# Optimization experiments

Measured on AMD Instinct MI355X. Metric: run time of the kernel, lower is better.

Reference implementation:

```python
import jax, jax.numpy as jnp
import numpy as np

B, S, QD, KD = 8, 8192, 1024, 1024
AD = min(QD, KD)
EPS = 1e-5


def _ste(x, xq):
    # straight-through estimator: forward uses xq, gradient flows as identity
    return x + jax.lax.stop_gradient(xq - x)


def bitlinear(x, w, b):
    """BitNet b1.58-style BitLinear: ternary per-tensor weight quant,
    per-token int8 absmax activation quant, both with STE."""
    s = jnp.mean(jnp.abs(w)) + EPS                      # per-tensor weight scale
    wq = _ste(w, jnp.clip(jnp.round(w / s), -1.0, 1.0) * s)
    g = jnp.max(jnp.abs(x), axis=-1, keepdims=True) + EPS  # per-token act scale
    xq = _ste(x, jnp.clip(jnp.round(x * (127.0 / g)), -128.0, 127.0) * (g / 127.0))
    return jnp.matmul(xq, wq.T) + b


def setup_inputs() -> dict:
    key = jax.random.key(0)
    ks = jax.random.split(key, 6)
    sc = 0.02
    return {
        "query": jax.random.normal(ks[0], (B, QD), dtype=jnp.float32),
        "context_memory": jax.random.normal(ks[1], (B, S, KD), dtype=jnp.float32),
        "w_q": jax.random.normal(ks[2], (AD, QD), dtype=jnp.float32) * sc,
        "b_q": jnp.zeros((AD,), dtype=jnp.float32),
        "w_k": jax.random.normal(ks[3], (AD, KD), dtype=jnp.float32) * sc,
        "b_k": jnp.zeros((AD,), dtype=jnp.float32),
        "w_v": jax.random.normal(ks[4], (QD, KD), dtype=jnp.float32) * sc,
        "b_v": jnp.zeros((QD,), dtype=jnp.float32),
        "w_c": jax.random.normal(ks[5], (QD, 2 * QD), dtype=jnp.float32) * sc,
        "b_c": jnp.zeros((QD,), dtype=jnp.float32),
    }


def reference(query, context_memory, w_q, b_q, w_k, b_k, w_v, b_v, w_c, b_c):
    attention_dim = w_q.shape[0]
    q = bitlinear(query, w_q, b_q)                 # [B, A]
    k = bitlinear(context_memory, w_k, b_k)        # [B, S, A]
    v = bitlinear(context_memory, w_v, b_v)        # [B, S, QD]
    scores = jnp.einsum('ba,bsa->bs', q, k) / (attention_dim ** 0.5)
    attn = jax.nn.softmax(scores, axis=-1)         # [B, S]
    ctx = jnp.einsum('bs,bsq->bq', attn, v)        # [B, QD]
    combined = jnp.concatenate([query, ctx], axis=-1)  # [B, 2*QD]
    return bitlinear(combined, w_c, b_c)           # [B, QD]
```

## Files before the change

kernel.cpp:

```cpp
#include <hip/hip_runtime.h>
#include <hip/hip_bf16.h>
#include <math.h>

#define EPS 1e-5f

static constexpr int Bb = 8;
static constexpr int Ss = 8192;
static constexpr int Dd = 1024;
static constexpr int NW = 128;
static constexpr int NWv = NW * 4;
static constexpr int TOK = Ss / NWv;
static constexpr int NCH = 64;
static constexpr int RC = Dd / NCH;


__device__ __forceinline__ float blk_reduce(float v, bool ismax, volatile float* lds) {
#pragma unroll
  for (int msk = 32; msk; msk >>= 1) {
    float o = __shfl_xor(v, msk);
    v = ismax ? fmaxf(v, o) : (v + o);
  }
  int w = threadIdx.x >> 6;
  __syncthreads();
  if ((threadIdx.x & 63) == 0) lds[w] = v;
  __syncthreads();
  return ismax ? fmaxf(fmaxf(lds[0], lds[1]), fmaxf(lds[2], lds[3]))
               : (lds[0] + lds[1] + lds[2] + lds[3]);
}

__device__ __forceinline__ float wred_max(float v) {
#pragma unroll
  for (int msk = 32; msk; msk >>= 1) v = fmaxf(v, __shfl_xor(v, msk));
  return v;
}

__device__ __forceinline__ float wred_sum(float v) {
#pragma unroll
  for (int msk = 32; msk; msk >>= 1) v += __shfl_xor(v, msk);
  return v;
}

__device__ __forceinline__ float quantf(float x, float c) {
  return fminf(fmaxf(rintf(x * c), -128.f), 127.f);
}

__device__ __forceinline__ float ternf(float w, float s) {
  return fminf(fmaxf(rintf(w / s), -1.f), 1.f);
}

__device__ __forceinline__ float4 tern4(float4 w, float s) {
  return make_float4(ternf(w.x, s), ternf(w.y, s), ternf(w.z, s), ternf(w.w, s));
}

__device__ __forceinline__ float4 quant4(float4 v, float c) {
  return make_float4(quantf(v.x, c), quantf(v.y, c), quantf(v.z, c), quantf(v.w, c));
}

__device__ __forceinline__ float absmax4(float4 v) {
  return fmaxf(fmaxf(fabsf(v.x), fabsf(v.y)), fmaxf(fabsf(v.z), fabsf(v.w)));
}


__global__ __launch_bounds__(256) void k_scales(
    const float* __restrict__ w0, const float* __restrict__ w1,
    const float* __restrict__ w2, const float* __restrict__ w3,
    double* __restrict__ part, float* __restrict__ scales, int* __restrict__ cnt)
{
  int seg = blockIdx.x >> 6;
  int blk = blockIdx.x & 63;
  const float* w = seg == 0 ? w0 : seg == 1 ? w1 : seg == 2 ? w2 : w3;
  int n4 = (seg == 3 ? (1024 * 2048) : (1024 * 1024)) >> 2;
  const float4* w4 = (const float4*)w;
  double acc = 0.0;
  for (int i = blk * 256 + threadIdx.x; i < n4; i += 64 * 256) {
    float4 v = w4[i];
    acc += (double)fabsf(v.x) + (double)fabsf(v.y)
         + (double)fabsf(v.z) + (double)fabsf(v.w);
  }
  __shared__ double sred[256];
  sred[threadIdx.x] = acc;
  __syncthreads();
  for (int s = 128; s > 0; s >>= 1) {
    if (threadIdx.x < s) sred[threadIdx.x] += sred[threadIdx.x + s];
    __syncthreads();
  }
  __shared__ int lastold;
  if (threadIdx.x == 0) {
    part[blockIdx.x] = sred[0];
    __threadfence();
    lastold = atomicAdd(cnt, 1);
  }
  __syncthreads();
  if (lastold == 255) {
    __threadfence();
    if (threadIdx.x < 4) {
      int sg = threadIdx.x;
      double s = 0.0;
      for (int i = 0; i < 64; i++) s += part[sg * 64 + i];
      double n = (sg == 3) ? 2097152.0 : 1048576.0;
      scales[sg] = (float)(s / n) + EPS;
    }
  }
}


__global__ __launch_bounds__(256) void k_qgemv(
    const float* __restrict__ query, const float* __restrict__ W,
    const float* __restrict__ bias, const float* __restrict__ scales,
    float* __restrict__ out)
{
  __shared__ float cs[Dd];
  __shared__ float red[4];
  int b = blockIdx.x >> 8, grp = blockIdx.x & 255;
  int tid = threadIdx.x, wv = tid >> 6, lane = tid & 63;
  float4 v = ((const float4*)(query + (size_t)b * Dd))[tid];
  float am = blk_reduce(absmax4(v), true, red);
  float g = am + EPS;
  float c = 127.0f / g;
  ((float4*)cs)[tid] = quant4(v, c);
  __syncthreads();
  float s = scales[0];
  int o = grp * 4 + wv;
  const float4* wr = (const float4*)(W + (size_t)o * Dd);
  float acc = 0.f;
#pragma unroll
  for (int i = 0; i < 4; i++) {
    int idx = i * 64 + lane;
    float4 w4 = wr[idx];
    float4 a4 = ((const float4*)cs)[idx];
    acc += a4.x * ternf(w4.x, s) + a4.y * ternf(w4.y, s)
         + a4.z * ternf(w4.z, s) + a4.w * ternf(w4.w, s);
  }
  acc = wred_sum(acc);
  if (lane == 0) out[(size_t)b * Dd + o] = s * (g / 127.0f) * acc + bias[o];
}


__global__ __launch_bounds__(256) void k_qk(
    const float* __restrict__ q, const float* __restrict__ Wk,
    const float* __restrict__ bk, const float* __restrict__ scales,
    float* __restrict__ part, float* __restrict__ qk, float* __restrict__ qdotbk,
    int* __restrict__ cnt)
{
  __shared__ float qs[Bb * RC];
  int ch = blockIdx.x;
  int a0 = ch * RC;
  int tid = threadIdx.x;
  if (tid < Bb * RC) {
    int b = tid / RC, a = tid - b * RC;
    qs[tid] = q[(size_t)b * Dd + a0 + a];
  }
  __syncthreads();
  float s = scales[1];
  float4 acc[Bb];
#pragma unroll
  for (int b = 0; b < Bb; b++) acc[b] = make_float4(0.f, 0.f, 0.f, 0.f);
  const float4* Wr = (const float4*)(Wk + (size_t)a0 * Dd);
  for (int i = 0; i < RC; i++) {
    float4 t4 = tern4(Wr[(size_t)i * 256 + tid], s);
#pragma unroll
    for (int b = 0; b < Bb; b++) {
      float qb = qs[b * RC + i];
      acc[b].x += qb * t4.x; acc[b].y += qb * t4.y;
      acc[b].z += qb * t4.z; acc[b].w += qb * t4.w;
    }
  }
#pragma unroll
  for (int b = 0; b < Bb; b++)
    ((float4*)part)[((size_t)ch * Bb + b) * 256 + tid] = acc[b];

  __threadfence();
  if (tid == 0) {
    atomicAdd(cnt, 1);
    while (__hip_atomic_load(cnt, __ATOMIC_ACQUIRE, __HIP_MEMORY_SCOPE_AGENT) < NCH)
      __builtin_amdgcn_s_sleep(8);
  }
  __syncthreads();
  __threadfence();

  int b = blockIdx.x >> 3, dc = blockIdx.x & 7;
  if (tid < 32) {
    int d4 = dc * 32 + tid;
    float4 a = make_float4(0.f, 0.f, 0.f, 0.f);
    for (int k = 0; k < NCH; k++) {
      float4 p = ((const float4*)part)[((size_t)k * Bb + b) * 256 + d4];
      a.x += p.x; a.y += p.y; a.z += p.z; a.w += p.w;
    }
    ((float4*)qk)[(size_t)b * 256 + d4] = make_float4(s * a.x, s * a.y, s * a.z, s * a.w);
  } else if (dc == 0 && tid >= 64 && tid < 128) {
    int lane = tid - 64;
    float p = 0.f;
    for (int a2 = lane; a2 < Dd; a2 += 64) p += q[(size_t)b * Dd + a2] * bk[a2];
    p = wred_sum(p);
    if (lane == 0) qdotbk[b] = p;
  }
}


__global__ __launch_bounds__(256) void k_pass(
    const float* __restrict__ X, const float* __restrict__ qk,
    const float* __restrict__ qdotbk,
    float* __restrict__ m_part, float* __restrict__ l_part,
    float* __restrict__ t_part)
{
  int b    = blockIdx.x >> 7;
  int wg   = blockIdx.x & 127;
  int wv   = threadIdx.x >> 6;
  int lane = threadIdx.x & 63;
  int widx = wg * 4 + wv;
  int s0   = widx * TOK;

  const float4* qkb = (const float4*)(qk + (size_t)b * Dd);
  float4 qv0 = qkb[lane], qv1 = qkb[64 + lane], qv2 = qkb[128 + lane], qv3 = qkb[192 + lane];
  float qb = qdotbk[b];
  const float4* Xw = (const float4*)(X + ((size_t)b * Ss + s0) * Dd);

  float m = -INFINITY, l = 0.f;
  float4 a0 = make_float4(0,0,0,0), a1 = a0, a2 = a0, a3 = a0;

  float4 x0 = Xw[lane], x1 = Xw[64 + lane], x2 = Xw[128 + lane], x3 = Xw[192 + lane];
  for (int i = 0; i < TOK; i++) {
    size_t nb = (size_t)((i + 1 < TOK) ? i + 1 : i) * 256;
    float4 n0 = Xw[nb + lane], n1 = Xw[nb + 64 + lane],
           n2 = Xw[nb + 128 + lane], n3 = Xw[nb + 192 + lane];

    float am = wred_max(fmaxf(fmaxf(absmax4(x0), absmax4(x1)),
                              fmaxf(absmax4(x2), absmax4(x3))));
    float g = am + EPS;
    float c = 127.0f / g;
    float gi = g / 127.0f;

    float q00 = rintf(x0.x * c), q01 = rintf(x0.y * c), q02 = rintf(x0.z * c), q03 = rintf(x0.w * c);
    float q10 = rintf(x1.x * c), q11 = rintf(x1.y * c), q12 = rintf(x1.z * c), q13 = rintf(x1.w * c);
    float q20 = rintf(x2.x * c), q21 = rintf(x2.y * c), q22 = rintf(x2.z * c), q23 = rintf(x2.w * c);
    float q30 = rintf(x3.x * c), q31 = rintf(x3.y * c), q32 = rintf(x3.z * c), q33 = rintf(x3.w * c);

    float dt = q00 * qv0.x + q01 * qv0.y + q02 * qv0.z + q03 * qv0.w
             + q10 * qv1.x + q11 * qv1.y + q12 * qv1.z + q13 * qv1.w
             + q20 * qv2.x + q21 * qv2.y + q22 * qv2.z + q23 * qv2.w
             + q30 * qv3.x + q31 * qv3.y + q32 * qv3.z + q33 * qv3.w;
    dt = wred_sum(dt);

    float score = (dt * gi + qb) * 0.03125f;
    if (score <= m) {
      float p  = __expf(score - m);
      l += p;
      float cf = p * gi;
      a0.x += cf * q00; a0.y += cf * q01; a0.z += cf * q02; a0.w += cf * q03;
      a1.x += cf * q10; a1.y += cf * q11; a1.z += cf * q12; a1.w += cf * q13;
      a2.x += cf * q20; a2.y += cf * q21; a2.z += cf * q22; a2.w += cf * q23;
      a3.x += cf * q30; a3.y += cf * q31; a3.z += cf * q32; a3.w += cf * q33;
    } else {
      float scl = __expf(m - score);
      l = l * scl + 1.0f;
      float cf = gi;
      a0.x = a0.x * scl + cf * q00; a0.y = a0.y * scl + cf * q01;
      a0.z = a0.z * scl + cf * q02; a0.w = a0.w * scl + cf * q03;
      a1.x = a1.x * scl + cf * q10; a1.y = a1.y * scl + cf * q11;
      a1.z = a1.z * scl + cf * q12; a1.w = a1.w * scl + cf * q13;
      a2.x = a2.x * scl + cf * q20; a2.y = a2.y * scl + cf * q21;
      a2.z = a2.z * scl + cf * q22; a2.w = a2.w * scl + cf * q23;
      a3.x = a3.x * scl + cf * q30; a3.y = a3.y * scl + cf * q31;
      a3.z = a3.z * scl + cf * q32; a3.w = a3.w * scl + cf * q33;
      m = score;
    }
    x0 = n0; x1 = n1; x2 = n2; x3 = n3;
  }

  size_t pidx = (size_t)b * NWv + widx;
  float4* tpw = (float4*)t_part + (size_t)pidx * 256;
  tpw[lane] = a0; tpw[64 + lane] = a1; tpw[128 + lane] = a2; tpw[192 + lane] = a3;
  if (lane == 0) { m_part[pidx] = m; l_part[pidx] = l; }
}


__global__ __launch_bounds__(256) void k_comb(
    const float* __restrict__ m_part, const float* __restrict__ l_part,
    const float* __restrict__ t_part, float* __restrict__ t16,
    float* __restrict__ t, int* __restrict__ cnt)
{
  __shared__ float red[4];
  int b = blockIdx.x >> 4, k = blockIdx.x & 15;
  int tid = threadIdx.x;
  float m1 = m_part[(size_t)b * NWv + tid];
  float m2 = m_part[(size_t)b * NWv + 256 + tid];
  float M = blk_reduce(fmaxf(m1, m2), true, red);
  float li = l_part[(size_t)b * NWv + tid] * __expf(m1 - M)
           + l_part[(size_t)b * NWv + 256 + tid] * __expf(m2 - M);
  float L = blk_reduce(li, false, red);

  float4 acc = make_float4(0,0,0,0);
  for (int i = 0; i < 32; i++) {
    size_t pi = (size_t)b * NWv + k * 32 + i;
    float w = __expf(m_part[pi] - M);
    float4 tp = ((const float4*)t_part)[pi * 256 + tid];
    acc.x += w * tp.x; acc.y += w * tp.y; acc.z += w * tp.z; acc.w += w * tp.w;
  }
  ((float4*)t16)[((size_t)(b * 16 + k)) * 256 + tid] = acc;

  __shared__ int lastold;
  if (tid == 0) {
    __threadfence();
    lastold = atomicAdd(&cnt[b], 1);
  }
  __syncthreads();
  if (lastold == 15) {
    __threadfence();
    float invL = 1.0f / L;
    float4 a = make_float4(0,0,0,0);
    for (int kk = 0; kk < 16; kk++) {
      float4 v = ((const float4*)t16)[((size_t)(b * 16 + kk)) * 256 + tid];
      a.x += v.x; a.y += v.y; a.z += v.z; a.w += v.w;
    }
    ((float4*)t)[(size_t)b * 256 + tid] =
        make_float4(a.x * invL, a.y * invL, a.z * invL, a.w * invL);
  }
}


__global__ __launch_bounds__(256) void k_tern_gemv_f32(
    const float* __restrict__ act, const float* __restrict__ W,
    const float* __restrict__ bias, const float* __restrict__ scales, int sidx,
    float* __restrict__ out, int K, int N)
{
  int wave = blockIdx.x * 4 + (threadIdx.x >> 6);
  int lane = threadIdx.x & 63;
  int b = wave / N, o = wave - b * N;
  float s = scales[sidx];
  const float4* wr = (const float4*)(W + (size_t)o * K);
  const float4* ar = (const float4*)(act + (size_t)b * K);
  int n4 = K >> 2;
  float acc = 0.f;
  for (int i = lane; i < n4; i += 64) {
    float4 w4 = wr[i];
    float4 a4 = ar[i];
    acc += a4.x * ternf(w4.x, s) + a4.y * ternf(w4.y, s)
         + a4.z * ternf(w4.z, s) + a4.w * ternf(w4.w, s);
  }
  acc = wred_sum(acc);
  if (lane == 0) out[(size_t)b * N + o] = s * acc + bias[o];
}


__global__ __launch_bounds__(256) void k_final(
    const float* __restrict__ query, const float* __restrict__ ctx,
    const float* __restrict__ W, const float* __restrict__ bias,
    const float* __restrict__ scales, float* __restrict__ out)
{
  __shared__ float cs[2 * Dd];
  __shared__ float red[4];
  int b = blockIdx.x >> 8, grp = blockIdx.x & 255;
  int tid = threadIdx.x, wv = tid >> 6, lane = tid & 63;
  float4 vq = ((const float4*)(query + (size_t)b * Dd))[tid];
  float4 vc = ((const float4*)(ctx   + (size_t)b * Dd))[tid];
  float am = blk_reduce(fmaxf(absmax4(vq), absmax4(vc)), true, red);
  float g = am + EPS;
  float c = 127.0f / g;
  ((float4*)cs)[tid]       = quant4(vq, c);
  ((float4*)cs)[256 + tid] = quant4(vc, c);
  __syncthreads();
  float s = scales[3];
  int o = grp * 4 + wv;
  const float4* wr = (const float4*)(W + (size_t)o * 2 * Dd);
  float acc = 0.f;
#pragma unroll
  for (int i = 0; i < 8; i++) {
    int idx = i * 64 + lane;
    float4 w4 = wr[idx];
    float4 a4 = ((const float4*)cs)[idx];
    acc += a4.x * ternf(w4.x, s) + a4.y * ternf(w4.y, s)
         + a4.z * ternf(w4.z, s) + a4.w * ternf(w4.w, s);
  }
  acc = wred_sum(acc);
  if (lane == 0) out[(size_t)b * Dd + o] = s * (g / 127.0f) * acc + bias[o];
}


extern "C" void kernel_launch(void* const* d_in, const int* in_sizes, int n_in,
                              void* d_out, int out_size, void* d_ws, size_t ws_size,
                              hipStream_t stream)
{
  const float* query = (const float*)d_in[0];
  const float* X     = (const float*)d_in[1];
  const float* w_q   = (const float*)d_in[2];
  const float* b_q   = (const float*)d_in[3];
  const float* w_k   = (const float*)d_in[4];
  const float* b_k   = (const float*)d_in[5];
  const float* w_v   = (const float*)d_in[6];
  const float* b_v   = (const float*)d_in[7];
  const float* w_c   = (const float*)d_in[8];
  const float* b_c   = (const float*)d_in[9];
  float* out = (float*)d_out;
  char* ws = (char*)d_ws;

  size_t off = 0;
  auto alloc = [&](size_t bytes) -> size_t {
    size_t o = off;
    off += (bytes + 255) & ~(size_t)255;
    return o;
  };
  size_t o_cnt    = alloc(256);
  size_t o_part   = alloc(256 * sizeof(double));
  size_t o_scales = alloc(4 * sizeof(float));
  size_t o_q      = alloc((size_t)Bb * Dd * 4);
  size_t o_qk     = alloc((size_t)Bb * Dd * 4);
  size_t o_qbk    = alloc(Bb * sizeof(float));
  size_t o_t      = alloc((size_t)Bb * Dd * 4);
  size_t o_ctx    = alloc((size_t)Bb * Dd * 4);
  size_t o_t16    = alloc((size_t)Bb * 16 * Dd * 4);
  size_t o_qkp    = alloc((size_t)NCH * Bb * Dd * 4);
  size_t o_mp     = alloc((size_t)Bb * NWv * 4);
  size_t o_lp     = alloc((size_t)Bb * NWv * 4);
  size_t o_tp     = alloc((size_t)Bb * NWv * Dd * 4);
  (void)ws_size;

  int*    cnt    = (int*)(ws + o_cnt);
  double* part   = (double*)(ws + o_part);
  float*  scales = (float*)(ws + o_scales);
  float*  qv     = (float*)(ws + o_q);
  float*  qk     = (float*)(ws + o_qk);
  float*  qbk    = (float*)(ws + o_qbk);
  float*  tvec   = (float*)(ws + o_t);
  float*  ctx    = (float*)(ws + o_ctx);
  float*  t16    = (float*)(ws + o_t16);
  float*  qkp    = (float*)(ws + o_qkp);
  float*  mp     = (float*)(ws + o_mp);
  float*  lp     = (float*)(ws + o_lp);
  float*  tp     = (float*)(ws + o_tp);

  hipMemsetAsync(ws + o_cnt, 0, 256, stream);
  k_scales<<<256, 256, 0, stream>>>(w_q, w_k, w_v, w_c, part, scales, &cnt[0]);
  k_qgemv<<<Bb * 256, 256, 0, stream>>>(query, w_q, b_q, scales, qv);
  k_qk<<<NCH, 256, 0, stream>>>(qv, w_k, b_k, scales, qkp, qk, qbk, &cnt[1]);
  k_pass<<<Bb * NW, 256, 0, stream>>>(X, qk, qbk, mp, lp, tp);
  k_comb<<<Bb * 16, 256, 0, stream>>>(mp, lp, tp, t16, tvec, &cnt[2]);
  k_tern_gemv_f32<<<(Bb * Dd) / 4, 256, 0, stream>>>(tvec, w_v, b_v, scales, 2, ctx, Dd, Dd);
  k_final<<<Bb * 256, 256, 0, stream>>>(query, ctx, w_c, b_c, scales, out);
}
```

Measured before the change: 142.0 us.

## Process token pairs per iteration and halve pass workgroups

```diff
diff --git a/kernel.cpp b/kernel.cpp
--- a/kernel.cpp
+++ b/kernel.cpp
@@ -7,9 +7,10 @@
 static constexpr int Bb = 8;
 static constexpr int Ss = 8192;
 static constexpr int Dd = 1024;
-static constexpr int NW = 128;
+static constexpr int NW = 64;
 static constexpr int NWv = NW * 4;
 static constexpr int TOK = Ss / NWv;
+static constexpr int NPAIR = TOK / 2;
 static constexpr int NCH = 64;
 static constexpr int RC = Dd / NCH;
 
@@ -26,12 +27,6 @@
   __syncthreads();
   return ismax ? fmaxf(fmaxf(lds[0], lds[1]), fmaxf(lds[2], lds[3]))
                : (lds[0] + lds[1] + lds[2] + lds[3]);
-}
-
-__device__ __forceinline__ float wred_max(float v) {
-#pragma unroll
-  for (int msk = 32; msk; msk >>= 1) v = fmaxf(v, __shfl_xor(v, msk));
-  return v;
 }
 
 __device__ __forceinline__ float wred_sum(float v) {
@@ -203,8 +198,8 @@
     float* __restrict__ m_part, float* __restrict__ l_part,
     float* __restrict__ t_part)
 {
-  int b    = blockIdx.x >> 7;
-  int wg   = blockIdx.x & 127;
+  int b    = blockIdx.x >> 6;
+  int wg   = blockIdx.x & 63;
   int wv   = threadIdx.x >> 6;
   int lane = threadIdx.x & 63;
   int widx = wg * 4 + wv;
@@ -218,53 +213,75 @@
   float m = -INFINITY, l = 0.f;
   float4 a0 = make_float4(0,0,0,0), a1 = a0, a2 = a0, a3 = a0;
 
-  float4 x0 = Xw[lane], x1 = Xw[64 + lane], x2 = Xw[128 + lane], x3 = Xw[192 + lane];
-  for (int i = 0; i < TOK; i++) {
-    size_t nb = (size_t)((i + 1 < TOK) ? i + 1 : i) * 256;
-    float4 n0 = Xw[nb + lane], n1 = Xw[nb + 64 + lane],
-           n2 = Xw[nb + 128 + lane], n3 = Xw[nb + 192 + lane];
-
-    float am = wred_max(fmaxf(fmaxf(absmax4(x0), absmax4(x1)),
-                              fmaxf(absmax4(x2), absmax4(x3))));
-    float g = am + EPS;
-    float c = 127.0f / g;
-    float gi = g / 127.0f;
-
-    float q00 = rintf(x0.x * c), q01 = rintf(x0.y * c), q02 = rintf(x0.z * c), q03 = rintf(x0.w * c);
-    float q10 = rintf(x1.x * c), q11 = rintf(x1.y * c), q12 = rintf(x1.z * c), q13 = rintf(x1.w * c);
-    float q20 = rintf(x2.x * c), q21 = rintf(x2.y * c), q22 = rintf(x2.z * c), q23 = rintf(x2.w * c);
-    float q30 = rintf(x3.x * c), q31 = rintf(x3.y * c), q32 = rintf(x3.z * c), q33 = rintf(x3.w * c);
-
-    float dt = q00 * qv0.x + q01 * qv0.y + q02 * qv0.z + q03 * qv0.w
-             + q10 * qv1.x + q11 * qv1.y + q12 * qv1.z + q13 * qv1.w
-             + q20 * qv2.x + q21 * qv2.y + q22 * qv2.z + q23 * qv2.w
-             + q30 * qv3.x + q31 * qv3.y + q32 * qv3.z + q33 * qv3.w;
-    dt = wred_sum(dt);
-
-    float score = (dt * gi + qb) * 0.03125f;
-    if (score <= m) {
-      float p  = __expf(score - m);
-      l += p;
-      float cf = p * gi;
-      a0.x += cf * q00; a0.y += cf * q01; a0.z += cf * q02; a0.w += cf * q03;
-      a1.x += cf * q10; a1.y += cf * q11; a1.z += cf * q12; a1.w += cf * q13;
-      a2.x += cf * q20; a2.y += cf * q21; a2.z += cf * q22; a2.w += cf * q23;
-      a3.x += cf * q30; a3.y += cf * q31; a3.z += cf * q32; a3.w += cf * q33;
-    } else {
-      float scl = __expf(m - score);
-      l = l * scl + 1.0f;
-      float cf = gi;
-      a0.x = a0.x * scl + cf * q00; a0.y = a0.y * scl + cf * q01;
-      a0.z = a0.z * scl + cf * q02; a0.w = a0.w * scl + cf * q03;
-      a1.x = a1.x * scl + cf * q10; a1.y = a1.y * scl + cf * q11;
-      a1.z = a1.z * scl + cf * q12; a1.w = a1.w * scl + cf * q13;
-      a2.x = a2.x * scl + cf * q20; a2.y = a2.y * scl + cf * q21;
-      a2.z = a2.z * scl + cf * q22; a2.w = a2.w * scl + cf * q23;
-      a3.x = a3.x * scl + cf * q30; a3.y = a3.y * scl + cf * q31;
-      a3.z = a3.z * scl + cf * q32; a3.w = a3.w * scl + cf * q33;
-      m = score;
-    }
-    x0 = n0; x1 = n1; x2 = n2; x3 = n3;
+  float4 xA0 = Xw[lane],       xA1 = Xw[64 + lane],  xA2 = Xw[128 + lane], xA3 = Xw[192 + lane];
+  float4 xB0 = Xw[256 + lane], xB1 = Xw[320 + lane], xB2 = Xw[384 + lane], xB3 = Xw[448 + lane];
+
+  for (int p = 0; p < NPAIR; p++) {
+    size_t nb = (size_t)((p + 1 < NPAIR) ? p + 1 : p) * 512;
+    float4 nA0 = Xw[nb + lane],       nA1 = Xw[nb + 64 + lane],
+           nA2 = Xw[nb + 128 + lane], nA3 = Xw[nb + 192 + lane];
+    float4 nB0 = Xw[nb + 256 + lane], nB1 = Xw[nb + 320 + lane],
+           nB2 = Xw[nb + 384 + lane], nB3 = Xw[nb + 448 + lane];
+
+    float amA = fmaxf(fmaxf(absmax4(xA0), absmax4(xA1)), fmaxf(absmax4(xA2), absmax4(xA3)));
+    float amB = fmaxf(fmaxf(absmax4(xB0), absmax4(xB1)), fmaxf(absmax4(xB2), absmax4(xB3)));
+#pragma unroll
+    for (int msk = 32; msk; msk >>= 1) {
+      float oA = __shfl_xor(amA, msk);
+      float oB = __shfl_xor(amB, msk);
+      amA = fmaxf(amA, oA);
+      amB = fmaxf(amB, oB);
+    }
+    float gA = amA + EPS, gB = amB + EPS;
+    float cA = 127.0f / gA, cB = 127.0f / gB;
+    float giA = gA / 127.0f, giB = gB / 127.0f;
+
+    float qA00 = quantf(xA0.x, cA), qA01 = quantf(xA0.y, cA), qA02 = quantf(xA0.z, cA), qA03 = quantf(xA0.w, cA);
+    float qA10 = quantf(xA1.x, cA), qA11 = quantf(xA1.y, cA), qA12 = quantf(xA1.z, cA), qA13 = quantf(xA1.w, cA);
+    float qA20 = quantf(xA2.x, cA), qA21 = quantf(xA2.y, cA), qA22 = quantf(xA2.z, cA), qA23 = quantf(xA2.w, cA);
+    float qA30 = quantf(xA3.x, cA), qA31 = quantf(xA3.y, cA), qA32 = quantf(xA3.z, cA), qA33 = quantf(xA3.w, cA);
+    float qB00 = quantf(xB0.x, cB), qB01 = quantf(xB0.y, cB), qB02 = quantf(xB0.z, cB), qB03 = quantf(xB0.w, cB);
+    float qB10 = quantf(xB1.x, cB), qB11 = quantf(xB1.y, cB), qB12 = quantf(xB1.z, cB), qB13 = quantf(xB1.w, cB);
+    float qB20 = quantf(xB2.x, cB), qB21 = quantf(xB2.y, cB), qB22 = quantf(xB2.z, cB), qB23 = quantf(xB2.w, cB);
+    float qB30 = quantf(xB3.x, cB), qB31 = quantf(xB3.y, cB), qB32 = quantf(xB3.z, cB), qB33 = quantf(xB3.w, cB);
+
+    float dtA = qA00 * qv0.x + qA01 * qv0.y + qA02 * qv0.z + qA03 * qv0.w
+              + qA10 * qv1.x + qA11 * qv1.y + qA12 * qv1.z + qA13 * qv1.w
+              + qA20 * qv2.x + qA21 * qv2.y + qA22 * qv2.z + qA23 * qv2.w
+              + qA30 * qv3.x + qA31 * qv3.y + qA32 * qv3.z + qA33 * qv3.w;
+    float dtB = qB00 * qv0.x + qB01 * qv0.y + qB02 * qv0.z + qB03 * qv0.w
+              + qB10 * qv1.x + qB11 * qv1.y + qB12 * qv1.z + qB13 * qv1.w
+              + qB20 * qv2.x + qB21 * qv2.y + qB22 * qv2.z + qB23 * qv2.w
+              + qB30 * qv3.x + qB31 * qv3.y + qB32 * qv3.z + qB33 * qv3.w;
+#pragma unroll
+    for (int msk = 32; msk; msk >>= 1) {
+      float oA = __shfl_xor(dtA, msk);
+      float oB = __shfl_xor(dtB, msk);
+      dtA += oA;
+      dtB += oB;
+    }
+
+    float sA = (dtA * giA + qb) * 0.03125f;
+    float sB = (dtB * giB + qb) * 0.03125f;
+
+    float mn  = fmaxf(m, fmaxf(sA, sB));
+    float scl = __expf(m - mn);
+    float eA  = __expf(sA - mn);
+    float eB  = __expf(sB - mn);
+    l = l * scl + eA + eB;
+    float cfA = eA * giA, cfB = eB * giB;
+    a0.x = a0.x * scl + cfA * qA00 + cfB * qB00; a0.y = a0.y * scl + cfA * qA01 + cfB * qB01;
+    a0.z = a0.z * scl + cfA * qA02 + cfB * qB02; a0.w = a0.w * scl + cfA * qA03 + cfB * qB03;
+    a1.x = a1.x * scl + cfA * qA10 + cfB * qB10; a1.y = a1.y * scl + cfA * qA11 + cfB * qB11;
+    a1.z = a1.z * scl + cfA * qA12 + cfB * qB12; a1.w = a1.w * scl + cfA * qA13 + cfB * qB13;
+    a2.x = a2.x * scl + cfA * qA20 + cfB * qB20; a2.y = a2.y * scl + cfA * qA21 + cfB * qB21;
+    a2.z = a2.z * scl + cfA * qA22 + cfB * qB22; a2.w = a2.w * scl + cfA * qA23 + cfB * qB23;
+    a3.x = a3.x * scl + cfA * qA30 + cfB * qB30; a3.y = a3.y * scl + cfA * qA31 + cfB * qB31;
+    a3.z = a3.z * scl + cfA * qA32 + cfB * qB32; a3.w = a3.w * scl + cfA * qA33 + cfB * qB33;
+    m = mn;
+
+    xA0 = nA0; xA1 = nA1; xA2 = nA2; xA3 = nA3;
+    xB0 = nB0; xB1 = nB1; xB2 = nB2; xB3 = nB3;
   }
 
   size_t pidx = (size_t)b * NWv + widx;
@@ -282,17 +299,15 @@
   __shared__ float red[4];
   int b = blockIdx.x >> 4, k = blockIdx.x & 15;
   int tid = threadIdx.x;
-  float m1 = m_part[(size_t)b * NWv + tid];
-  float m2 = m_part[(size_t)b * NWv + 256 + tid];
-  float M = blk_reduce(fmaxf(m1, m2), true, red);
-  float li = l_part[(size_t)b * NWv + tid] * __expf(m1 - M)
-           + l_part[(size_t)b * NWv + 256 + tid] * __expf(m2 - M);
+  float mi = m_part[(size_t)b * NWv + tid];
+  float M = blk_reduce(mi, true, red);
+  float li = l_part[(size_t)b * NWv + tid] * expf(mi - M);
   float L = blk_reduce(li, false, red);
 
   float4 acc = make_float4(0,0,0,0);
-  for (int i = 0; i < 32; i++) {
-    size_t pi = (size_t)b * NWv + k * 32 + i;
-    float w = __expf(m_part[pi] - M);
+  for (int i = 0; i < 16; i++) {
+    size_t pi = (size_t)b * NWv + k * 16 + i;
+    float w = expf(m_part[pi] - M);
     float4 tp = ((const float4*)t_part)[pi * 256 + tid];
     acc.x += w * tp.x; acc.y += w * tp.y; acc.z += w * tp.z; acc.w += w * tp.w;
   }
```

Measured after the change: 134.7 us. 5.1% less time.
